# Optimization experiments

Measured on AMD Instinct MI355X. Metric: run time of the kernel, lower is better.

The kernel has to match this reference:

```python
import jax, jax.numpy as jnp
import numpy as np

OUT = 7          # roi_align output_size
NUM_ANCHORS = 27 # 3 scales x 3 ratios x 3 angles
MAX_PROPOSALS = 100
RPN_STRIDE = 32


def conv2d(x, w, b, stride=1, pad=1):
    y = jax.lax.conv_general_dilated(
        x, w, (stride, stride), [(pad, pad), (pad, pad)],
        dimension_numbers=('NCHW', 'OIHW', 'NCHW'))
    return y + b[None, :, None, None]


def generate_anchors(H, W, stride):
    # matches CustomOrientedRPN.generate_anchors
    sx = np.arange(0, W * stride, stride, dtype=np.float32)
    sy = np.arange(0, H * stride, stride, dtype=np.float32)
    SY, SX = np.meshgrid(sy, sx, indexing='ij')
    shifts = np.stack([SX, SY], axis=-1).reshape(-1, 2)  # [HW,2]
    base = []
    for scale in (32.0, 64.0, 128.0):
        for ratio in (0.5, 1.0, 2.0):
            w = scale * ratio ** 0.5
            h = scale / ratio ** 0.5
            for angle in (0.0, 45.0, 90.0):
                base.append([w, h, angle])
    base = np.array(base, dtype=np.float32)  # [A,3]
    A = base.shape[0]
    anchors = np.concatenate(
        [np.repeat(shifts[:, None, :], A, axis=1),
         np.broadcast_to(base[None], (shifts.shape[0], A, 3))], axis=-1)
    return jnp.asarray(anchors.reshape(-1, 5))  # [HW*A, 5]


def rotated_roi_align(features, boxes, batch_idx):
    # Vectorized version of the per-box affine_grid + grid_sample loop
    # (align_corners=False semantics for both, zero padding for grid_sample).
    B, C, Hf, Wf = features.shape
    lin = (2.0 * jnp.arange(OUT, dtype=features.dtype) + 1.0) / OUT - 1.0
    ys, xs = jnp.meshgrid(lin, lin, indexing='ij')  # [7,7] base grid

    cx, cy, w, h, ang = (boxes[:, i] for i in range(5))
    ar = -ang * jnp.pi / 180.0
    c, s = jnp.cos(ar), jnp.sin(ar)
    t00 = w / Wf * c; t01 = -h / Hf * s; t02 = 2.0 * cx / Wf - 1.0
    t10 = w / Wf * s; t11 = h / Hf * c;  t12 = 2.0 * cy / Hf - 1.0
    gx = t00[:, None, None] * xs + t01[:, None, None] * ys + t02[:, None, None]  # [N,7,7]
    gy = t10[:, None, None] * xs + t11[:, None, None] * ys + t12[:, None, None]

    ix = ((gx + 1.0) * Wf - 1.0) / 2.0
    iy = ((gy + 1.0) * Hf - 1.0) / 2.0
    x0 = jnp.floor(ix); y0 = jnp.floor(iy)
    wx = ix - x0;       wy = iy - y0
    x0i = x0.astype(jnp.int32); y0i = y0.astype(jnp.int32)

    def gather(dx, dy, wgt):
        xi = x0i + dx; yi = y0i + dy
        valid = (xi >= 0) & (xi < Wf) & (yi >= 0) & (yi < Hf)
        xc = jnp.clip(xi, 0, Wf - 1)
        yc = jnp.clip(yi, 0, Hf - 1)
        def one(bi, yb, xb):
            return features[bi][:, yb, xb]  # [C,7,7]
        vals = jax.vmap(one)(batch_idx, yc, xc)  # [N,C,7,7]
        return vals * (wgt * valid)[:, None, :, :]

    return (gather(0, 0, (1 - wx) * (1 - wy)) + gather(1, 0, wx * (1 - wy)) +
            gather(0, 1, (1 - wx) * wy) + gather(1, 1, wx * wy))


def setup_inputs() -> dict:
    key = jax.random.key(0)
    ks = jax.random.split(key, 20)

    def w(k, shape):
        fan_in = int(np.prod(shape[1:]))
        return jax.random.normal(k, shape, jnp.float32) / np.sqrt(fan_in)

    C = 256; A = NUM_ANCHORS; NC = 5
    return {
        'images': jax.random.normal(ks[0], (8, 3, 1024, 1024), jnp.float32),
        'backbone_w': w(ks[1], (C, 3, 3, 3)),   'backbone_b': jnp.zeros((C,), jnp.float32),
        'rpn_conv_w': w(ks[2], (256, C, 3, 3)), 'rpn_conv_b': jnp.zeros((256,), jnp.float32),
        'obj_w': w(ks[3], (A, 256, 1, 1)),      'obj_b': jnp.zeros((A,), jnp.float32),
        'delta_w': w(ks[4], (A * 5, 256, 1, 1)) * 0.1, 'delta_b': jnp.zeros((A * 5,), jnp.float32),
        'fc1_w': w(ks[5], (1024, C * OUT * OUT)), 'fc1_b': jnp.zeros((1024,), jnp.float32),
        'fc2_w': w(ks[6], (1024, 1024)),          'fc2_b': jnp.zeros((1024,), jnp.float32),
        'cls_w': w(ks[7], (NC, 1024)),            'cls_b': jnp.zeros((NC,), jnp.float32),
        'bbox_w': w(ks[8], (5, 1024)),            'bbox_b': jnp.zeros((5,), jnp.float32),
    }


def reference(images, backbone_w, backbone_b, rpn_conv_w, rpn_conv_b,
              obj_w, obj_b, delta_w, delta_b,
              fc1_w, fc1_b, fc2_w, fc2_b, cls_w, cls_b, bbox_w, bbox_b):
    # backbone (stand-in: single stride-16 conv)
    f = conv2d(images, backbone_w, backbone_b, stride=16, pad=1)  # [B,256,64,64]
    B, C, H, W = f.shape
    # F.interpolate(scale_factor=0.5, bilinear, align_corners=False) == 2x2 mean
    f = f.reshape(B, C, H // 2, 2, W // 2, 2).mean(axis=(3, 5))   # [B,256,32,32]
    Hf, Wf = f.shape[2], f.shape[3]

    # RPN
    t = jax.nn.relu(conv2d(f, rpn_conv_w, rpn_conv_b, 1, 1))
    _logits = conv2d(t, obj_w, obj_b, 1, 0)  # computed as in original (unused downstream)
    deltas = conv2d(t, delta_w, delta_b, 1, 0)  # [B, A*5, Hf, Wf]
    A = NUM_ANCHORS
    deltas = deltas.reshape(B, A, 5, Hf, Wf).transpose(0, 3, 4, 1, 2).reshape(B, -1, 5)

    anchors = generate_anchors(Hf, Wf, RPN_STRIDE)  # [HW*A,5]
    acx, acy, aw, ah, aa = (anchors[:, i] for i in range(5))
    pcx = deltas[:, :, 0] * aw + acx
    pcy = deltas[:, :, 1] * ah + acy
    pw = jnp.exp(deltas[:, :, 2]) * aw
    ph = jnp.exp(deltas[:, :, 3]) * ah
    pa = aa + deltas[:, :, 4]
    proposals = jnp.stack([pcx, pcy, pw, ph, pa], axis=-1)  # [B, HW*A, 5]
    proposals = proposals[:, :MAX_PROPOSALS]                # p[:max_proposals]

    boxes = proposals.reshape(-1, 5)                        # [B*100, 5]
    batch_idx = jnp.repeat(jnp.arange(B), MAX_PROPOSALS)
    pooled = rotated_roi_align(f, boxes, batch_idx)         # [B*100, 256, 7, 7]

    x = pooled.reshape(pooled.shape[0], -1)
    x = jax.nn.relu(x @ fc1_w.T + fc1_b)
    x = jax.nn.relu(x @ fc2_w.T + fc2_b)
    class_logits = x @ cls_w.T + cls_b
    obb_preds = x @ bbox_w.T + bbox_b
    return class_logits, obb_preds
```

## Files before the change

### kernel.cpp

```cpp
#include <hip/hip_runtime.h>
#include <hip/hip_bf16.h>

using bf16 = __hip_bfloat16;

typedef __attribute__((ext_vector_type(8))) short bf16x8;
typedef __attribute__((ext_vector_type(4))) float f32x4;

__device__ __forceinline__ void async16(const void* g, void* l) {
  __builtin_amdgcn_global_load_lds(
      (const __attribute__((address_space(1))) unsigned int*)g,
      (__attribute__((address_space(3))) unsigned int*)l, 16, 0, 0);
}

__device__ __forceinline__ void store_o(float* C, size_t i, float v) { C[i] = v; }
__device__ __forceinline__ void store_o(bf16* C, size_t i, float v) {
  C[i] = __float2bfloat16(v);
}

__global__ __launch_bounds__(256) void k_backbone(const float* __restrict__ img,
    const float* __restrict__ w, const float* __restrict__ bias,
    float* __restrict__ f) {
  int blk = blockIdx.x;
  int x = blk & 31, y = (blk >> 5) & 31, b = blk >> 10;
  __shared__ float patch[4 * 27];
  int t = threadIdx.x;
  if (t < 108) {
    int kx = t % 3, ky = (t / 3) % 3, cin = (t / 9) % 3, sub = t / 27;
    int sy = sub >> 1, sx = sub & 1;
    int iy = (2 * y + sy) * 16 - 1 + ky;
    int ix = (2 * x + sx) * 16 - 1 + kx;
    float v = 0.f;
    if (iy >= 0 && ix >= 0)
      v = img[((size_t)(b * 3 + cin) * 1024 + iy) * 1024 + ix];
    patch[t] = v;
  }
  __syncthreads();
  int c = t;
  float wr[27];
#pragma unroll
  for (int k = 0; k < 27; ++k) wr[k] = w[c * 27 + k];
  float acc = 0.f;
#pragma unroll
  for (int sub = 0; sub < 4; ++sub)
#pragma unroll
    for (int k = 0; k < 27; ++k)
      acc += patch[sub * 27 + k] * wr[k];
  f[(size_t)blk * 256 + c] = acc * 0.25f + bias[c];
}

__global__ __launch_bounds__(256) void k_rpn(const float* __restrict__ f,
    const float* __restrict__ rpn_w, float* __restrict__ part) {
  int p = blockIdx.x;
  int kc = blockIdx.y;
  int x = p & 3, b = p >> 2;
  __shared__ float fpl[6][16];
  int tid = threadIdx.x;
  if (tid < 96) {
    int cin2 = tid & 15;
    int rc = tid >> 4;
    int row = rc / 3, col = rc % 3;
    int xc = x - 1 + col;
    float v = 0.f;
    if (xc >= 0)
      v = f[((size_t)(b * 32 + row) * 32 + xc) * 256 + kc * 16 + cin2];
    fpl[rc][cin2] = v;
  }
  __syncthreads();
  int c = tid;
  const float* wbase = rpn_w + (size_t)c * 2304 + kc * 144;
  float acc = 0.f;
#pragma unroll
  for (int cin2 = 0; cin2 < 16; ++cin2) {
    const float* wp = wbase + cin2 * 9;
    acc += fpl[0][cin2] * wp[3] + fpl[1][cin2] * wp[4]
         + fpl[2][cin2] * wp[5] + fpl[3][cin2] * wp[6]
         + fpl[4][cin2] * wp[7] + fpl[5][cin2] * wp[8];
  }
  part[((size_t)kc * 32 + p) * 256 + c] = acc;
}

__global__ __launch_bounds__(512) void k_delta(const float* __restrict__ part,
    const float* __restrict__ rpn_b,
    const float* __restrict__ dw, const float* __restrict__ db,
    float* __restrict__ boxes) {
  int p = blockIdx.x;
  int x = p & 3, b = p >> 2;
  __shared__ float tbuf[256];
  __shared__ float dvals[135];
  int tid = threadIdx.x;
  if (tid < 256) {
    float s = rpn_b[tid];
#pragma unroll
    for (int kc = 0; kc < 16; ++kc)
      s += part[((size_t)kc * 32 + p) * 256 + tid];
    tbuf[tid] = fmaxf(s, 0.f);
  }
  __syncthreads();
  if (tid < 270) {
    int o = tid >> 1, half = tid & 1;
    const float* wp = dw + (size_t)o * 256 + half * 128;
    const float* tp = tbuf + half * 128;
    float s = 0.f;
#pragma unroll 8
    for (int k = 0; k < 128; ++k) s += tp[k] * wp[k];
    s += __shfl_xor(s, 1, 64);
    if (half == 0) dvals[o] = s + db[o];
  }
  __syncthreads();
  if (tid < 27) {
    int i = x * 27 + tid;
    if (i < 100) {
      int a = tid;
      int si = a / 9, ri = (a / 3) % 3, ai = a % 3;
      float scale = 32.f * (float)(1 << si);
      float sr = (ri == 0) ? 0.70710678118654752f : (ri == 1 ? 1.0f : 1.41421356237309505f);
      float aw = scale * sr, ah = scale / sr;
      float aang = 45.f * (float)ai;
      float acx = 32.f * (float)x, acy = 0.f;
      float* bx = boxes + (size_t)(b * 100 + i) * 5;
      bx[0] = dvals[a * 5 + 0] * aw + acx;
      bx[1] = dvals[a * 5 + 1] * ah + acy;
      bx[2] = expf(dvals[a * 5 + 2]) * aw;
      bx[3] = expf(dvals[a * 5 + 3]) * ah;
      bx[4] = aang + dvals[a * 5 + 4];
    }
  }
}

__global__ __launch_bounds__(256) void k_roialign(const float* __restrict__ f,
    const float* __restrict__ boxes, bf16* __restrict__ pooled) {
  int n = blockIdx.x;
  int b = n / 100;
  __shared__ int six[49], siy[49];
  __shared__ float swx[49], swy[49];
  __shared__ float pool_s[12544];
  int tid = threadIdx.x;
  if (tid < 49) {
    float cx = boxes[n * 5 + 0], cy = boxes[n * 5 + 1];
    float w = boxes[n * 5 + 2], h = boxes[n * 5 + 3], ang = boxes[n * 5 + 4];
    float ar = -ang * 0.017453292519943295f;
    float cc = cosf(ar), ss = sinf(ar);
    float t00 = w * (1.f / 32.f) * cc, t01 = -h * (1.f / 32.f) * ss;
    float t02 = cx * (2.f / 32.f) - 1.f;
    float t10 = w * (1.f / 32.f) * ss, t11 = h * (1.f / 32.f) * cc;
    float t12 = cy * (2.f / 32.f) - 1.f;
    int py = tid / 7, px = tid - py * 7;
    float lx = (2.f * px + 1.f) * (1.f / 7.f) - 1.f;
    float ly = (2.f * py + 1.f) * (1.f / 7.f) - 1.f;
    float gx = t00 * lx + t01 * ly + t02;
    float gy = t10 * lx + t11 * ly + t12;
    float ix = ((gx + 1.f) * 32.f - 1.f) * 0.5f;
    float iy = ((gy + 1.f) * 32.f - 1.f) * 0.5f;
    float x0 = floorf(ix), y0 = floorf(iy);
    six[tid] = (int)x0; siy[tid] = (int)y0;
    swx[tid] = ix - x0; swy[tid] = iy - y0;
  }
  __syncthreads();
  const float* fb = f + (size_t)b * 262144;
  int c = tid;
  for (int bin = 0; bin < 49; ++bin) {
    int x0 = six[bin], y0 = siy[bin];
    float wx = swx[bin], wy = swy[bin];
    float acc = 0.f;
    if (x0 >= 0 && x0 < 32 && y0 >= 0 && y0 < 32)
      acc += fb[(y0 * 32 + x0) * 256 + c] * ((1.f - wx) * (1.f - wy));
    if (x0 + 1 >= 0 && x0 + 1 < 32 && y0 >= 0 && y0 < 32)
      acc += fb[(y0 * 32 + x0 + 1) * 256 + c] * (wx * (1.f - wy));
    if (x0 >= 0 && x0 < 32 && y0 + 1 >= 0 && y0 + 1 < 32)
      acc += fb[((y0 + 1) * 32 + x0) * 256 + c] * ((1.f - wx) * wy);
    if (x0 + 1 >= 0 && x0 + 1 < 32 && y0 + 1 >= 0 && y0 + 1 < 32)
      acc += fb[((y0 + 1) * 32 + x0 + 1) * 256 + c] * (wx * wy);
    pool_s[c * 49 + bin] = acc;
  }
  __syncthreads();
  bf16* po = pooled + (size_t)n * 12544;
  for (int k = tid; k < 12544; k += 256) po[k] = __float2bfloat16(pool_s[k]);
}

__global__ __launch_bounds__(256) void k_gemm_sk(
    const unsigned short* __restrict__ A, const float* __restrict__ B,
    float* __restrict__ P, int M, int N, int K, int KC) {
  __shared__ unsigned short As[128 * 64];
  __shared__ unsigned short Bs[64 * 72];
  int t = threadIdx.x;
  int wv = t >> 6, ln = t & 63;
  int quad = ln >> 4, l15 = ln & 15;
  int wm = wv >> 1, wn = wv & 1;
  int n0 = blockIdx.x * 64, m0 = blockIdx.y * 128;
  int kbeg = blockIdx.z * KC;
  int kend = kbeg + KC; if (kend > K) kend = K;

  int srow = ln >> 3;
  int sg = (ln & 7) ^ srow;
  const unsigned short* Ap[4];
#pragma unroll
  for (int q = 0; q < 4; ++q) {
    int r = m0 + q * 32 + wv * 8 + srow;
    if (r > M - 1) r = M - 1;
    Ap[q] = A + (size_t)r * K + sg * 8;
  }

  int brow = t >> 2, bq = t & 3;
  const float* Bp = B + (size_t)(n0 + brow) * K + bq * 16;
  unsigned short* bdst = &Bs[brow * 72 + bq * 16];

  f32x4 acc[4][2];
#pragma unroll
  for (int mf = 0; mf < 4; ++mf)
#pragma unroll
    for (int nf = 0; nf < 2; ++nf) acc[mf][nf] = (f32x4){0.f, 0.f, 0.f, 0.f};

  for (int k0 = kbeg; k0 < kend; k0 += 64) {
    float4 bv0 = *(const float4*)(Bp + k0);
    float4 bv1 = *(const float4*)(Bp + k0 + 4);
    float4 bv2 = *(const float4*)(Bp + k0 + 8);
    float4 bv3 = *(const float4*)(Bp + k0 + 12);
    __syncthreads();
#pragma unroll
    for (int q = 0; q < 4; ++q)
      async16(Ap[q] + k0, &As[q * 2048 + wv * 512]);
    unsigned short bb[16];
    bb[0]  = __bfloat16_as_ushort(__float2bfloat16(bv0.x));
    bb[1]  = __bfloat16_as_ushort(__float2bfloat16(bv0.y));
    bb[2]  = __bfloat16_as_ushort(__float2bfloat16(bv0.z));
    bb[3]  = __bfloat16_as_ushort(__float2bfloat16(bv0.w));
    bb[4]  = __bfloat16_as_ushort(__float2bfloat16(bv1.x));
    bb[5]  = __bfloat16_as_ushort(__float2bfloat16(bv1.y));
    bb[6]  = __bfloat16_as_ushort(__float2bfloat16(bv1.z));
    bb[7]  = __bfloat16_as_ushort(__float2bfloat16(bv1.w));
    bb[8]  = __bfloat16_as_ushort(__float2bfloat16(bv2.x));
    bb[9]  = __bfloat16_as_ushort(__float2bfloat16(bv2.y));
    bb[10] = __bfloat16_as_ushort(__float2bfloat16(bv2.z));
    bb[11] = __bfloat16_as_ushort(__float2bfloat16(bv2.w));
    bb[12] = __bfloat16_as_ushort(__float2bfloat16(bv3.x));
    bb[13] = __bfloat16_as_ushort(__float2bfloat16(bv3.y));
    bb[14] = __bfloat16_as_ushort(__float2bfloat16(bv3.z));
    bb[15] = __bfloat16_as_ushort(__float2bfloat16(bv3.w));
#pragma unroll
    for (int u = 0; u < 2; ++u)
      *(bf16x8*)(bdst + u * 8) = *(const bf16x8*)(bb + u * 8);
    __syncthreads();
#pragma unroll
    for (int ks = 0; ks < 2; ++ks) {
      bf16x8 a[4];
#pragma unroll
      for (int mf = 0; mf < 4; ++mf) {
        int row = wm * 64 + mf * 16 + l15;
        a[mf] = *(const bf16x8*)&As[row * 64 + (((ks * 4 + quad) ^ (l15 & 7)) * 8)];
      }
#pragma unroll
      for (int nf = 0; nf < 2; ++nf) {
        bf16x8 b = *(const bf16x8*)&Bs[(wn * 32 + nf * 16 + l15) * 72 + ks * 32 + quad * 8];
#pragma unroll
        for (int mf = 0; mf < 4; ++mf)
          acc[mf][nf] = __builtin_amdgcn_mfma_f32_16x16x32_bf16(a[mf], b, acc[mf][nf], 0, 0, 0);
      }
    }
  }
  float* Pz = P + (size_t)blockIdx.z * M * N;
#pragma unroll
  for (int nf = 0; nf < 2; ++nf) {
    int n = n0 + wn * 32 + nf * 16 + l15;
#pragma unroll
    for (int mf = 0; mf < 4; ++mf) {
#pragma unroll
      for (int r = 0; r < 4; ++r) {
        int m = m0 + wm * 64 + mf * 16 + quad * 4 + r;
        if (m < M) Pz[(size_t)m * N + n] = acc[mf][nf][r];
      }
    }
  }
}

template <typename OutT, int KS>
__global__ __launch_bounds__(256) void k_reduce(const float* __restrict__ P,
    const float* __restrict__ bias, OutT* __restrict__ C, int MN, int N) {
  int i = blockIdx.x * 256 + threadIdx.x;
  if (i * 4 >= MN) return;
  f32x4 s = *(const f32x4*)(P + (size_t)i * 4);
#pragma unroll
  for (int z = 1; z < KS; ++z)
    s += *(const f32x4*)(P + (size_t)z * MN + i * 4);
  int n = (i * 4) % N;
#pragma unroll
  for (int u = 0; u < 4; ++u)
    store_o(C, (size_t)i * 4 + u, fmaxf(s[u] + bias[n + u], 0.f));
}

__global__ __launch_bounds__(640) void k_heads(const float* __restrict__ x2,
    const float* __restrict__ cls_w, const float* __restrict__ cls_b,
    const float* __restrict__ bbox_w, const float* __restrict__ bbox_b,
    float* __restrict__ out) {
  int n = blockIdx.x;
  int wave = threadIdx.x >> 6;
  int lane = threadIdx.x & 63;
  const float* w = (wave < 5) ? (cls_w + (size_t)wave * 1024)
                              : (bbox_w + (size_t)(wave - 5) * 1024);
  const float* xr = x2 + (size_t)n * 1024;
  float s = 0.f;
  for (int k = lane; k < 1024; k += 64) s += xr[k] * w[k];
  for (int off = 32; off; off >>= 1) s += __shfl_down(s, off, 64);
  if (lane == 0) {
    int o = (wave < 5) ? wave : wave - 5;
    float bias = (wave < 5) ? cls_b[o] : bbox_b[o];
    int base = (wave < 5) ? 0 : 4000;
    out[base + n * 5 + o] = s + bias;
  }
}

extern "C" void kernel_launch(void* const* d_in, const int* in_sizes, int n_in,
                              void* d_out, int out_size, void* d_ws, size_t ws_size,
                              hipStream_t stream) {
  const float* images     = (const float*)d_in[0];
  const float* backbone_w = (const float*)d_in[1];
  const float* backbone_b = (const float*)d_in[2];
  const float* rpn_w      = (const float*)d_in[3];
  const float* rpn_b      = (const float*)d_in[4];
  const float* delta_w    = (const float*)d_in[7];
  const float* delta_b    = (const float*)d_in[8];
  const float* fc1_w      = (const float*)d_in[9];
  const float* fc1_b      = (const float*)d_in[10];
  const float* fc2_w      = (const float*)d_in[11];
  const float* fc2_b      = (const float*)d_in[12];
  const float* cls_w      = (const float*)d_in[13];
  const float* cls_b      = (const float*)d_in[14];
  const float* bbox_w     = (const float*)d_in[15];
  const float* bbox_b     = (const float*)d_in[16];

  char* ws = (char*)d_ws;
  float* f      = (float*)ws;
  float* boxes  = (float*)(ws + 8388608);
  bf16*  pooled = (bf16*) (ws + 8404992);
  bf16*  x1     = (bf16*) (ws + 28475392);
  float* x2     = (float*)(ws + 30113792);
  float* parts  = (float*)(ws + 33390592);
  float* rpart = parts;

  k_backbone<<<8192, 256, 0, stream>>>(images, backbone_w, backbone_b, f);
  k_rpn<<<dim3(32, 16), 256, 0, stream>>>(f, rpn_w, rpart);
  k_delta<<<32, 512, 0, stream>>>(rpart, rpn_b, delta_w, delta_b, boxes);
  k_roialign<<<800, 256, 0, stream>>>(f, boxes, pooled);

  k_gemm_sk<<<dim3(16, 7, 6), 256, 0, stream>>>(
      (const unsigned short*)pooled, fc1_w, parts, 800, 1024, 12544, 2112);
  k_reduce<bf16, 6><<<800, 256, 0, stream>>>(parts, fc1_b, x1, 819200, 1024);

  k_gemm_sk<<<dim3(16, 7, 4), 256, 0, stream>>>(
      (const unsigned short*)x1, fc2_w, parts, 800, 1024, 1024, 256);
  k_reduce<float, 4><<<800, 256, 0, stream>>>(parts, fc2_b, x2, 819200, 1024);

  k_heads<<<800, 640, 0, stream>>>(x2, cls_w, cls_b, bbox_w, bbox_b, (float*)d_out);
}
```

Baseline: 336.4 us.

## Double-buffer split-K GEMM shared-memory tiles to overlap loads with MFMA

Gives the split-K GEMM kernel two shared-memory buffers for the A and B tiles. The next K-tile is prefetched (async global-to-LDS for A, register loads plus bf16 conversion for B) while MFMAs run on the current tile, leaving one barrier per iteration instead of two. The aim is to hide global memory latency behind compute, at the cost of doubling LDS use, which may lower occupancy.

Result: slower. 343.8 us (+2.2%).

```diff
diff --git a/kernel.cpp b/kernel.cpp
--- a/kernel.cpp
+++ b/kernel.cpp
@@ -180,8 +180,8 @@
 __global__ __launch_bounds__(256) void k_gemm_sk(
     const unsigned short* __restrict__ A, const float* __restrict__ B,
     float* __restrict__ P, int M, int N, int K, int KC) {
-  __shared__ unsigned short As[128 * 64];
-  __shared__ unsigned short Bs[64 * 72];
+  __shared__ unsigned short As[2][128 * 64];
+  __shared__ unsigned short Bs[2][64 * 72];
   int t = threadIdx.x;
   int wv = t >> 6, ln = t & 63;
   int quad = ln >> 4, l15 = ln & 15;
@@ -202,7 +202,6 @@
 
   int brow = t >> 2, bq = t & 3;
   const float* Bp = B + (size_t)(n0 + brow) * K + bq * 16;
-  unsigned short* bdst = &Bs[brow * 72 + bq * 16];
 
   f32x4 acc[4][2];
 #pragma unroll
@@ -210,53 +209,95 @@
 #pragma unroll
     for (int nf = 0; nf < 2; ++nf) acc[mf][nf] = (f32x4){0.f, 0.f, 0.f, 0.f};
 
-  for (int k0 = kbeg; k0 < kend; k0 += 64) {
-    float4 bv0 = *(const float4*)(Bp + k0);
-    float4 bv1 = *(const float4*)(Bp + k0 + 4);
-    float4 bv2 = *(const float4*)(Bp + k0 + 8);
-    float4 bv3 = *(const float4*)(Bp + k0 + 12);
-    __syncthreads();
+  {
+    float4 v0 = *(const float4*)(Bp + kbeg);
+    float4 v1 = *(const float4*)(Bp + kbeg + 4);
+    float4 v2 = *(const float4*)(Bp + kbeg + 8);
+    float4 v3 = *(const float4*)(Bp + kbeg + 12);
 #pragma unroll
     for (int q = 0; q < 4; ++q)
-      async16(Ap[q] + k0, &As[q * 2048 + wv * 512]);
+      async16(Ap[q] + kbeg, &As[0][q * 2048 + wv * 512]);
     unsigned short bb[16];
-    bb[0]  = __bfloat16_as_ushort(__float2bfloat16(bv0.x));
-    bb[1]  = __bfloat16_as_ushort(__float2bfloat16(bv0.y));
-    bb[2]  = __bfloat16_as_ushort(__float2bfloat16(bv0.z));
-    bb[3]  = __bfloat16_as_ushort(__float2bfloat16(bv0.w));
-    bb[4]  = __bfloat16_as_ushort(__float2bfloat16(bv1.x));
-    bb[5]  = __bfloat16_as_ushort(__float2bfloat16(bv1.y));
-    bb[6]  = __bfloat16_as_ushort(__float2bfloat16(bv1.z));
-    bb[7]  = __bfloat16_as_ushort(__float2bfloat16(bv1.w));
-    bb[8]  = __bfloat16_as_ushort(__float2bfloat16(bv2.x));
-    bb[9]  = __bfloat16_as_ushort(__float2bfloat16(bv2.y));
-    bb[10] = __bfloat16_as_ushort(__float2bfloat16(bv2.z));
-    bb[11] = __bfloat16_as_ushort(__float2bfloat16(bv2.w));
-    bb[12] = __bfloat16_as_ushort(__float2bfloat16(bv3.x));
-    bb[13] = __bfloat16_as_ushort(__float2bfloat16(bv3.y));
-    bb[14] = __bfloat16_as_ushort(__float2bfloat16(bv3.z));
-    bb[15] = __bfloat16_as_ushort(__float2bfloat16(bv3.w));
+    bb[0]  = __bfloat16_as_ushort(__float2bfloat16(v0.x));
+    bb[1]  = __bfloat16_as_ushort(__float2bfloat16(v0.y));
+    bb[2]  = __bfloat16_as_ushort(__float2bfloat16(v0.z));
+    bb[3]  = __bfloat16_as_ushort(__float2bfloat16(v0.w));
+    bb[4]  = __bfloat16_as_ushort(__float2bfloat16(v1.x));
+    bb[5]  = __bfloat16_as_ushort(__float2bfloat16(v1.y));
+    bb[6]  = __bfloat16_as_ushort(__float2bfloat16(v1.z));
+    bb[7]  = __bfloat16_as_ushort(__float2bfloat16(v1.w));
+    bb[8]  = __bfloat16_as_ushort(__float2bfloat16(v2.x));
+    bb[9]  = __bfloat16_as_ushort(__float2bfloat16(v2.y));
+    bb[10] = __bfloat16_as_ushort(__float2bfloat16(v2.z));
+    bb[11] = __bfloat16_as_ushort(__float2bfloat16(v2.w));
+    bb[12] = __bfloat16_as_ushort(__float2bfloat16(v3.x));
+    bb[13] = __bfloat16_as_ushort(__float2bfloat16(v3.y));
+    bb[14] = __bfloat16_as_ushort(__float2bfloat16(v3.z));
+    bb[15] = __bfloat16_as_ushort(__float2bfloat16(v3.w));
+    unsigned short* bdst = &Bs[0][brow * 72 + bq * 16];
 #pragma unroll
     for (int u = 0; u < 2; ++u)
       *(bf16x8*)(bdst + u * 8) = *(const bf16x8*)(bb + u * 8);
-    __syncthreads();
+  }
+  __syncthreads();
+
+  int buf = 0;
+  for (int k0 = kbeg; k0 < kend; k0 += 64) {
+    int k1 = k0 + 64;
+    int more = (k1 < kend);
+    float4 v0, v1, v2, v3;
+    if (more) {
+      v0 = *(const float4*)(Bp + k1);
+      v1 = *(const float4*)(Bp + k1 + 4);
+      v2 = *(const float4*)(Bp + k1 + 8);
+      v3 = *(const float4*)(Bp + k1 + 12);
+#pragma unroll
+      for (int q = 0; q < 4; ++q)
+        async16(Ap[q] + k1, &As[buf ^ 1][q * 2048 + wv * 512]);
+    }
 #pragma unroll
     for (int ks = 0; ks < 2; ++ks) {
       bf16x8 a[4];
 #pragma unroll
       for (int mf = 0; mf < 4; ++mf) {
         int row = wm * 64 + mf * 16 + l15;
-        a[mf] = *(const bf16x8*)&As[row * 64 + (((ks * 4 + quad) ^ (l15 & 7)) * 8)];
+        a[mf] = *(const bf16x8*)&As[buf][row * 64 + (((ks * 4 + quad) ^ (l15 & 7)) * 8)];
       }
 #pragma unroll
       for (int nf = 0; nf < 2; ++nf) {
-        bf16x8 b = *(const bf16x8*)&Bs[(wn * 32 + nf * 16 + l15) * 72 + ks * 32 + quad * 8];
+        bf16x8 b = *(const bf16x8*)&Bs[buf][(wn * 32 + nf * 16 + l15) * 72 + ks * 32 + quad * 8];
 #pragma unroll
         for (int mf = 0; mf < 4; ++mf)
           acc[mf][nf] = __builtin_amdgcn_mfma_f32_16x16x32_bf16(a[mf], b, acc[mf][nf], 0, 0, 0);
       }
     }
-  }
+    if (more) {
+      unsigned short bb[16];
+      bb[0]  = __bfloat16_as_ushort(__float2bfloat16(v0.x));
+      bb[1]  = __bfloat16_as_ushort(__float2bfloat16(v0.y));
+      bb[2]  = __bfloat16_as_ushort(__float2bfloat16(v0.z));
+      bb[3]  = __bfloat16_as_ushort(__float2bfloat16(v0.w));
+      bb[4]  = __bfloat16_as_ushort(__float2bfloat16(v1.x));
+      bb[5]  = __bfloat16_as_ushort(__float2bfloat16(v1.y));
+      bb[6]  = __bfloat16_as_ushort(__float2bfloat16(v1.z));
+      bb[7]  = __bfloat16_as_ushort(__float2bfloat16(v1.w));
+      bb[8]  = __bfloat16_as_ushort(__float2bfloat16(v2.x));
+      bb[9]  = __bfloat16_as_ushort(__float2bfloat16(v2.y));
+      bb[10] = __bfloat16_as_ushort(__float2bfloat16(v2.z));
+      bb[11] = __bfloat16_as_ushort(__float2bfloat16(v2.w));
+      bb[12] = __bfloat16_as_ushort(__float2bfloat16(v3.x));
+      bb[13] = __bfloat16_as_ushort(__float2bfloat16(v3.y));
+      bb[14] = __bfloat16_as_ushort(__float2bfloat16(v3.z));
+      bb[15] = __bfloat16_as_ushort(__float2bfloat16(v3.w));
+      unsigned short* bdst = &Bs[buf ^ 1][brow * 72 + bq * 16];
+#pragma unroll
+      for (int u = 0; u < 2; ++u)
+        *(bf16x8*)(bdst + u * 8) = *(const bf16x8*)(bb + u * 8);
+    }
+    __syncthreads();
+    buf ^= 1;
+  }
+
   float* Pz = P + (size_t)blockIdx.z * M * N;
 #pragma unroll
   for (int nf = 0; nf < 2; ++nf) {
```
